# Performance work log

Hardware: AMD Instinct MI355X
Metric: run time of the kernel (lower is better)

## Reference

```python
import jax, jax.numpy as jnp
import numpy as np

H_DIM = 2048
D_FF = 4 * H_DIM
NUM_EXPERTS = 8
NUM_SHARED = 2
BATCH, SEQ = 2, 2048


def setup_inputs() -> dict:
    key = jax.random.key(0)
    ks = jax.random.split(key, 10)
    s = 0.02
    return {
        "x": jax.random.normal(ks[0], (BATCH, SEQ, H_DIM), dtype=jnp.float32),
        "ws_w1": jax.random.normal(ks[1], (NUM_SHARED, H_DIM, D_FF), dtype=jnp.float32) * s,
        "ws_b1": jnp.zeros((NUM_SHARED, D_FF), dtype=jnp.float32),
        "ws_w2": jax.random.normal(ks[2], (NUM_SHARED, D_FF, H_DIM), dtype=jnp.float32) * s,
        "ws_b2": jnp.zeros((NUM_SHARED, H_DIM), dtype=jnp.float32),
        "we_w1": jax.random.normal(ks[3], (NUM_EXPERTS, H_DIM, D_FF), dtype=jnp.float32) * s,
        "we_b1": jnp.zeros((NUM_EXPERTS, D_FF), dtype=jnp.float32),
        "we_w2": jax.random.normal(ks[4], (NUM_EXPERTS, D_FF, H_DIM), dtype=jnp.float32) * s,
        "we_b2": jnp.zeros((NUM_EXPERTS, H_DIM), dtype=jnp.float32),
        "wg": jax.random.normal(ks[5], (H_DIM, NUM_EXPERTS), dtype=jnp.float32) * s,
        "top_k": 2,
    }


def reference(x, ws_w1, ws_b1, ws_w2, ws_b2, we_w1, we_b1, we_w2, we_b2, wg, top_k):
    B, S, D = x.shape
    xt = x.reshape(-1, D)  # [T, D], T = B*S
    T = xt.shape[0]

    # ---- shared experts: sum over NUM_SHARED dense MLPs ----
    hs = jax.nn.relu(jnp.einsum('td,ndf->ntf', xt, ws_w1) + ws_b1[:, None, :])
    shared = jnp.einsum('ntf,nfd->td', hs, ws_w2) + ws_b2.sum(axis=0)  # [T, D]

    # ---- sparse top-k routed MoE ----
    logits = xt @ wg                       # [T, E] router logits
    probs = jax.nn.softmax(logits, axis=-1)
    topv, topi = jax.lax.top_k(probs, top_k)
    gates = jnp.zeros_like(probs).at[jnp.arange(T)[:, None], topi].set(topv)  # [T, E]

    moe = jnp.zeros_like(xt)
    for e in range(we_w1.shape[0]):  # small fixed expert count
        he = jax.nn.relu(xt @ we_w1[e] + we_b1[e])
        ye = he @ we_w2[e] + we_b2[e]
        moe = moe + gates[:, e:e + 1] * ye

    out = (shared + moe).reshape(B, S, D)
    return out, logits
```

## Files before the change

kernel.cpp:

```cpp
#include <hip/hip_runtime.h>

#define TOKENS 4096
#define HD 2048
#define FF 8192
#define NE 8
#define NS 2

typedef __attribute__((ext_vector_type(8))) short bf16x8;
typedef __attribute__((ext_vector_type(4))) float f32x4;

__device__ __forceinline__ unsigned rnd_bf(unsigned u) {
  return u + 0x7fffu + ((u >> 16) & 1u);
}
__device__ __forceinline__ unsigned short f2bf(float f) {
  unsigned u = __builtin_bit_cast(unsigned, f);
  return (unsigned short)(rnd_bf(u) >> 16);
}

#define GLDS16(gp, lp)                                                         \
  __builtin_amdgcn_global_load_lds(                                            \
      (const __attribute__((address_space(1))) unsigned*)(const void*)(gp),    \
      (__attribute__((address_space(3))) unsigned*)(lp), 16, 0, 0)

__global__ void cast_x_kernel(const float* __restrict__ x, unsigned short* __restrict__ xb) {
  const size_t i = ((size_t)blockIdx.x * 256 + threadIdx.x) * 4;
  float4 v = *(const float4*)(x + i);
  ushort4 o;
  o.x = f2bf(v.x); o.y = f2bf(v.y); o.z = f2bf(v.z); o.w = f2bf(v.w);
  *(ushort4*)(xb + i) = o;
}

__global__ void router_kernel(const float* __restrict__ x, const float* __restrict__ wg,
                              float* __restrict__ logits_out, int* __restrict__ topi,
                              float* __restrict__ topv, int* __restrict__ counts) {
  const int wave = threadIdx.x >> 6, lane = threadIdx.x & 63;
  const int t = blockIdx.x * 4 + wave;
  const float* xr = x + (size_t)t * HD;
  float acc[8];
#pragma unroll
  for (int e = 0; e < 8; ++e) acc[e] = 0.f;
  for (int d = lane; d < HD; d += 64) {
    const float xv = xr[d];
    const float4 w0 = *(const float4*)(wg + (size_t)d * 8);
    const float4 w1 = *(const float4*)(wg + (size_t)d * 8 + 4);
    acc[0] += xv * w0.x; acc[1] += xv * w0.y; acc[2] += xv * w0.z; acc[3] += xv * w0.w;
    acc[4] += xv * w1.x; acc[5] += xv * w1.y; acc[6] += xv * w1.z; acc[7] += xv * w1.w;
  }
#pragma unroll
  for (int e = 0; e < 8; ++e) {
#pragma unroll
    for (int off = 32; off > 0; off >>= 1) acc[e] += __shfl_xor(acc[e], off);
  }
  if (lane == 0) {
    *(float4*)(logits_out + (size_t)t * 8)     = make_float4(acc[0], acc[1], acc[2], acc[3]);
    *(float4*)(logits_out + (size_t)t * 8 + 4) = make_float4(acc[4], acc[5], acc[6], acc[7]);
    float mx = acc[0];
#pragma unroll
    for (int e = 1; e < 8; ++e) mx = fmaxf(mx, acc[e]);
    float p[8], s = 0.f;
#pragma unroll
    for (int e = 0; e < 8; ++e) { p[e] = expf(acc[e] - mx); s += p[e]; }
    const float inv = 1.f / s;
    int i1 = 0;
#pragma unroll
    for (int e = 1; e < 8; ++e) if (acc[e] > acc[i1]) i1 = e;
    int i2 = (i1 == 0) ? 1 : 0;
#pragma unroll
    for (int e = 0; e < 8; ++e) if (e != i1 && acc[e] > acc[i2]) i2 = e;
    topi[2 * t]     = i1; topv[2 * t]     = p[i1] * inv;
    topi[2 * t + 1] = i2; topv[2 * t + 1] = p[i2] * inv;
    atomicAdd(&counts[i1], 1);
    atomicAdd(&counts[i2], 1);
  }
}

__global__ void offs_kernel(const int* __restrict__ counts, int* __restrict__ offs,
                            int* __restrict__ cursors) {
  if (threadIdx.x == 0) {
    int r = 0;
    for (int e = 0; e < NE; ++e) { offs[e] = r; cursors[e] = r; r += counts[e]; }
  }
}

__global__ void gather_kernel(const unsigned short* __restrict__ xb,
                              const int* __restrict__ topi, const float* __restrict__ topv,
                              int* __restrict__ cursors, unsigned short* __restrict__ xg,
                              int* __restrict__ row_token, float* __restrict__ row_gate) {
  const int wave = threadIdx.x >> 6, lane = threadIdx.x & 63;
  const int t = blockIdx.x * 4 + wave;
  const uint4* src = (const uint4*)(xb + (size_t)t * HD);
#pragma unroll
  for (int j = 0; j < 2; ++j) {
    const int e = topi[2 * t + j];
    int pos = 0;
    if (lane == 0) {
      pos = atomicAdd(&cursors[e], 1);
      row_token[pos] = t;
      row_gate[pos] = topv[2 * t + j];
    }
    pos = __shfl(pos, 0);
    uint4* dst = (uint4*)(xg + (size_t)pos * HD);
#pragma unroll
    for (int c = lane; c < 256; c += 64) dst[c] = src[c];
  }
}

template <int K, int N>
__global__ __launch_bounds__(256) void pack_wt(const float* __restrict__ we,
                                               const float* __restrict__ ws,
                                               unsigned short* __restrict__ dstw) {
  const int e = blockIdx.z;
  const float* src = (e < NE) ? (we + (size_t)e * K * N) : (ws + (size_t)(e - NE) * K * N);
  unsigned short* dst = dstw + (size_t)e * K * N;
  const int nt = blockIdx.x * 64;
  const int kt = blockIdx.y * 64;
  __shared__ unsigned short t[64][73];
  const int tid = threadIdx.x;
  const int rr = tid >> 4, cc = (tid & 15) * 4;
#pragma unroll
  for (int i = 0; i < 4; ++i) {
    const int k = rr + i * 16;
    float4 v = *(const float4*)(src + (size_t)(kt + k) * N + nt + cc);
    t[k][cc + 0] = f2bf(v.x);
    t[k][cc + 1] = f2bf(v.y);
    t[k][cc + 2] = f2bf(v.z);
    t[k][cc + 3] = f2bf(v.w);
  }
  __syncthreads();
  const int nr = tid >> 2, kc = (tid & 3) * 16;
  unsigned u[8];
#pragma unroll
  for (int j = 0; j < 8; ++j)
    u[j] = (unsigned)t[kc + 2 * j][nr] | ((unsigned)t[kc + 2 * j + 1][nr] << 16);
  unsigned short* dp = dst + (size_t)(nt + nr) * K + kt + kc;
  uint4 v0; v0.x = u[0]; v0.y = u[1]; v0.z = u[2]; v0.w = u[3];
  uint4 v1; v1.x = u[4]; v1.y = u[5]; v1.z = u[6]; v1.w = u[7];
  *(uint4*)dp = v0;
  *(uint4*)(dp + 8) = v1;
}

template <int MS>
__device__ __forceinline__ void rd_a(bf16x8 (&d)[8], const unsigned short* base,
                                     int wr, int fr, int fq, int swz) {
#pragma unroll
  for (int mi = 0; mi < 4; ++mi)
#pragma unroll
    for (int ks = 0; ks < 2; ++ks)
      d[mi * 2 + ks] = *(const bf16x8*)(base + (wr * 128 + MS * 64 + mi * 16 + fr) * 64 +
                                        (((ks * 4 + fq) ^ swz) << 3));
}
template <int NSUB>
__device__ __forceinline__ void rd_b(bf16x8 (&d)[4], const unsigned short* base,
                                     int wc, int fr, int fq, int swz) {
#pragma unroll
  for (int ni = 0; ni < 2; ++ni)
#pragma unroll
    for (int ks = 0; ks < 2; ++ks)
      d[ni * 2 + ks] = *(const bf16x8*)(base + (wc * 64 + NSUB * 32 + ni * 16 + fr) * 64 +
                                        (((ks * 4 + fq) ^ swz) << 3));
}
template <int MS, int NSUB>
__device__ __forceinline__ void mm16(f32x4 (&acc)[8][4], const bf16x8 (&a)[8],
                                     const bf16x8 (&b)[4]) {
  __builtin_amdgcn_s_setprio(1);
#pragma unroll
  for (int mi = 0; mi < 4; ++mi)
#pragma unroll
    for (int ni = 0; ni < 2; ++ni)
#pragma unroll
      for (int ks = 0; ks < 2; ++ks)
        acc[MS * 4 + mi][NSUB * 2 + ni] = __builtin_amdgcn_mfma_f32_16x16x32_bf16(
            a[mi * 2 + ks], b[ni * 2 + ks], acc[MS * 4 + mi][NSUB * 2 + ni], 0, 0, 0);
  __builtin_amdgcn_s_setprio(0);
}

template <int MODE>
__global__ __launch_bounds__(512, 2) void gemm8p(
    const unsigned short* __restrict__ Ash,
    const unsigned short* __restrict__ Art,
    const unsigned short* __restrict__ wt,
    const float* __restrict__ bE, const float* __restrict__ bS,
    unsigned short* __restrict__ hout, float* __restrict__ out,
    const int* __restrict__ counts, const int* __restrict__ offs,
    const int* __restrict__ row_token, const float* __restrict__ row_gate) {
  constexpr int K = (MODE == 0) ? HD : FF;
  constexpr int N = (MODE == 0) ? FF : HD;
  constexpr int NBX = N / 256;
  constexpr int NWG = NBX * 16;
  extern __shared__ unsigned short smem[];

  const int e = blockIdx.z;
  int M;
  const unsigned short* A;
  const float* bias;
  int hbase = 0;
  const int* tok = nullptr;
  const float* gt = nullptr;

  if (e < NE) {
    M = counts[e];
    const int off = offs[e];
    A = Art + (size_t)off * K;
    if (MODE == 1) { tok = row_token + off; gt = row_gate + off; }
    bias = bE + (size_t)e * N;
    hbase = off;
  } else {
    M = TOKENS;
    const int se = e - NE;
    hbase = 2 * TOKENS + se * TOKENS;
    if (MODE == 0) A = Ash;
    else           A = Ash + (size_t)hbase * K;
    bias = bS + (size_t)se * N;
  }
  const unsigned short* Bt = wt + (size_t)e * HD * FF;

  int flat = blockIdx.x + NBX * blockIdx.y;
  flat = (flat & 7) * (NWG >> 3) + (flat >> 3);
  const int m0 = (flat & 15) * 256;
  const int n0 = (flat >> 4) * 256;
  if (m0 >= M) return;

  const int tid = threadIdx.x;
  const int wid = tid >> 6, ln = tid & 63;
  const int wr = wid >> 2, wc = wid & 3;
  const int fr = ln & 15, fq = ln >> 4;
  const int swz = fr & 7;

  const int srr = tid >> 3;
  const int soct = tid & 7;
  const int scol = (soct ^ (srr & 7)) << 3;

#define STAGE_A(h, kt, b)                                                      \
  { const unsigned short* s_ = A + (size_t)(m0 + (h) * 128 + srr) * K + (kt) * 64 + scol; \
    unsigned short* d_ = smem + (b) * 32768 + ((h) * 128 + srr) * 64 + soct * 8; \
    GLDS16(s_, d_); GLDS16(s_ + (size_t)64 * K, d_ + 4096); }
#define STAGE_B(h, kt, b)                                                      \
  { const unsigned short* s_ = Bt + (size_t)(n0 + (h) * 128 + srr) * K + (kt) * 64 + scol; \
    unsigned short* d_ = smem + (b) * 32768 + 16384 + ((h) * 128 + srr) * 64 + soct * 8; \
    GLDS16(s_, d_); GLDS16(s_ + (size_t)64 * K, d_ + 4096); }

  f32x4 acc[8][4];
#pragma unroll
  for (int i = 0; i < 8; ++i)
#pragma unroll
    for (int j = 0; j < 4; ++j) acc[i][j] = (f32x4){0.f, 0.f, 0.f, 0.f};

  STAGE_A(0, 0, 0); STAGE_B(0, 0, 0); STAGE_A(1, 0, 0); STAGE_B(1, 0, 0);
  STAGE_B(0, 1, 1); STAGE_A(0, 1, 1);
  asm volatile("s_waitcnt vmcnt(4)" ::: "memory");
  __builtin_amdgcn_s_barrier();

  bf16x8 a0[8], a1[8], b0[4], b1[4];
  const int nkt = K / 64;
  int cur = 0;
  for (int t = 0; t < nkt; ++t) {
    const int nxt = cur ^ 1;
    const int tp1 = (t + 1 < nkt) ? t + 1 : t;
    const int tp2 = (t + 2 < nkt) ? t + 2 : t;
    const unsigned short* As_c = smem + cur * 32768;
    const unsigned short* Bs_c = As_c + 16384;
    rd_a<0>(a0, As_c, wr, fr, fq, swz);
    rd_b<0>(b0, Bs_c, wc, fr, fq, swz);
    STAGE_A(1, tp1, nxt);
    __builtin_amdgcn_s_barrier();
    mm16<0, 0>(acc, a0, b0);
    __builtin_amdgcn_s_barrier();
    rd_b<1>(b1, Bs_c, wc, fr, fq, swz);
    STAGE_B(1, tp1, nxt);
    __builtin_amdgcn_s_barrier();
    mm16<0, 1>(acc, a0, b1);
    __builtin_amdgcn_s_barrier();
    rd_a<1>(a1, As_c, wr, fr, fq, swz);
    STAGE_B(0, tp2, cur);
    __builtin_amdgcn_s_barrier();
    mm16<1, 1>(acc, a1, b1);
    __builtin_amdgcn_s_barrier();
    STAGE_A(0, tp2, cur);
    __builtin_amdgcn_s_barrier();
    mm16<1, 0>(acc, a1, b0);
    asm volatile("s_waitcnt vmcnt(4)" ::: "memory");
    __builtin_amdgcn_s_barrier();
    cur = nxt;
  }
#undef STAGE_A
#undef STAGE_B

  if (MODE == 0) {
#pragma unroll
    for (int nn = 0; nn < 4; ++nn) {
      const int col = n0 + wc * 64 + (nn >> 1) * 32 + (nn & 1) * 16 + fr;
      const float bb = bias[col];
#pragma unroll
      for (int mm = 0; mm < 8; ++mm) {
#pragma unroll
        for (int j = 0; j < 4; ++j) {
          const int r = m0 + wr * 128 + (mm >> 2) * 64 + (mm & 3) * 16 + fq * 4 + j;
          if (r < M) {
            float v = acc[mm][nn][j] + bb;
            v = v > 0.f ? v : 0.f;
            hout[(size_t)(hbase + r) * FF + col] = f2bf(v);
          }
        }
      }
    }
  } else {
#pragma unroll
    for (int mm = 0; mm < 8; ++mm) {
#pragma unroll
      for (int j = 0; j < 4; ++j) {
        const int r = m0 + wr * 128 + (mm >> 2) * 64 + (mm & 3) * 16 + fq * 4 + j;
        if (r < M) {
          const int t = tok ? tok[r] : r;
          const float g = gt ? gt[r] : 1.f;
          float* orow = out + (size_t)t * HD + n0;
#pragma unroll
          for (int nn = 0; nn < 4; ++nn) {
            const int col = wc * 64 + (nn >> 1) * 32 + (nn & 1) * 16 + fr;
            atomicAdd(orow + col, g * (acc[mm][nn][j] + bias[n0 + col]));
          }
        }
      }
    }
  }
}

extern "C" void kernel_launch(void* const* d_in, const int* in_sizes, int n_in,
                              void* d_out, int out_size, void* d_ws, size_t ws_size,
                              hipStream_t stream) {
  const float* x     = (const float*)d_in[0];
  const float* ws_w1 = (const float*)d_in[1];
  const float* ws_b1 = (const float*)d_in[2];
  const float* ws_w2 = (const float*)d_in[3];
  const float* ws_b2 = (const float*)d_in[4];
  const float* we_w1 = (const float*)d_in[5];
  const float* we_b1 = (const float*)d_in[6];
  const float* we_w2 = (const float*)d_in[7];
  const float* we_b2 = (const float*)d_in[8];
  const float* wg    = (const float*)d_in[9];

  float* out = (float*)d_out;
  float* logits = out + (size_t)TOKENS * HD;

  char* ws = (char*)d_ws;
  unsigned short* wt   = (unsigned short*)ws;
  unsigned short* xb   = (unsigned short*)(ws + 335544320);
  unsigned short* xg   = (unsigned short*)(ws + 352321536);
  unsigned short* hbuf = (unsigned short*)(ws + 386400256);
  char* ctrl = ws + 654835712;
  int*   row_token = (int*)(ctrl);
  float* row_gate  = (float*)(ctrl + 32768);
  int*   topi      = (int*)(ctrl + 65536);
  float* topv      = (float*)(ctrl + 98304);
  int*   counts    = (int*)(ctrl + 131072);
  int*   offs      = (int*)(ctrl + 131104);
  int*   cursors   = (int*)(ctrl + 131136);

  hipFuncSetAttribute(reinterpret_cast<const void*>(gemm8p<0>),
                      hipFuncAttributeMaxDynamicSharedMemorySize, 131072);
  hipFuncSetAttribute(reinterpret_cast<const void*>(gemm8p<1>),
                      hipFuncAttributeMaxDynamicSharedMemorySize, 131072);

  hipMemsetAsync(out, 0, (size_t)TOKENS * HD * sizeof(float), stream);
  hipMemsetAsync(counts, 0, NE * sizeof(int), stream);

  cast_x_kernel<<<8192, 256, 0, stream>>>(x, xb);
  router_kernel<<<1024, 256, 0, stream>>>(x, wg, logits, topi, topv, counts);
  offs_kernel<<<1, 64, 0, stream>>>(counts, offs, cursors);
  gather_kernel<<<1024, 256, 0, stream>>>(xb, topi, topv, cursors, xg, row_token, row_gate);

  pack_wt<HD, FF><<<dim3(FF / 64, HD / 64, 10), 256, 0, stream>>>(we_w1, ws_w1, wt);
  gemm8p<0><<<dim3(32, 16, 10), 512, 131072, stream>>>(
      xb, xg, wt, we_b1, ws_b1, hbuf, nullptr, counts, offs, nullptr, nullptr);
  pack_wt<FF, HD><<<dim3(HD / 64, FF / 64, 10), 256, 0, stream>>>(we_w2, ws_w2, wt);
  gemm8p<1><<<dim3(8, 16, 10), 512, 131072, stream>>>(
      hbuf, hbuf, wt, we_b2, ws_b2, nullptr, out, counts, offs, row_token, row_gate);

  (void)in_sizes; (void)n_in; (void)out_size; (void)ws_size;
}
```

Before: 2.019 ms.

## Restage GEMM tiles per-wave with full two-tile-ahead prefetch pipeline

Changes how global-to-LDS loads are assigned: each wave now loads the rows it will itself read (wave-local row groups with 8-row strides), instead of a block-wide 128-row split. The prefetch schedule becomes uniform: both halves of A and B for tile t+2 are issued into the current buffer during compute of tile t, with a deeper vmcnt(8) wait. This aims to reduce cross-wave dependencies and smooth memory issue across the loop. The cost is more outstanding loads and registers, plus the risk of buffer overwrite hazards if the barriers do not fully cover reads of the current buffer.

```diff
diff --git a/kernel.cpp b/kernel.cpp
--- a/kernel.cpp
+++ b/kernel.cpp
@@ -226,18 +226,22 @@
   const int fr = ln & 15, fq = ln >> 4;
   const int swz = fr & 7;
 
-  const int srr = tid >> 3;
-  const int soct = tid & 7;
-  const int scol = (soct ^ (srr & 7)) << 3;
-
-#define STAGE_A(h, kt, b)                                                      \
-  { const unsigned short* s_ = A + (size_t)(m0 + (h) * 128 + srr) * K + (kt) * 64 + scol; \
-    unsigned short* d_ = smem + (b) * 32768 + ((h) * 128 + srr) * 64 + soct * 8; \
-    GLDS16(s_, d_); GLDS16(s_ + (size_t)64 * K, d_ + 4096); }
-#define STAGE_B(h, kt, b)                                                      \
-  { const unsigned short* s_ = Bt + (size_t)(n0 + (h) * 128 + srr) * K + (kt) * 64 + scol; \
-    unsigned short* d_ = smem + (b) * 32768 + 16384 + ((h) * 128 + srr) * 64 + soct * 8; \
-    GLDS16(s_, d_); GLDS16(s_ + (size_t)64 * K, d_ + 4096); }
+  const int lr8 = ln >> 3;
+  const int lc8 = ln & 7;
+  const int scol = (lc8 ^ lr8) << 3;
+  const int wrA = wr * 128 + wc * 16;
+  const int wcB = wc * 64 + wr * 16;
+
+#define SA(s, kt, b)                                                           \
+  { const int r0_ = wrA + (s) * 64 + lr8;                                      \
+    const unsigned short* s_ = A + (size_t)(m0 + r0_) * K + (kt) * 64 + scol;  \
+    unsigned short* d_ = smem + (b) * 32768 + r0_ * 64 + lc8 * 8;              \
+    GLDS16(s_, d_); GLDS16(s_ + (size_t)8 * K, d_ + 8 * 64); }
+#define SB(s, kt, b)                                                           \
+  { const int r0_ = wcB + (s) * 32 + lr8;                                      \
+    const unsigned short* s_ = Bt + (size_t)(n0 + r0_) * K + (kt) * 64 + scol; \
+    unsigned short* d_ = smem + (b) * 32768 + 16384 + r0_ * 64 + lc8 * 8;      \
+    GLDS16(s_, d_); GLDS16(s_ + (size_t)8 * K, d_ + 8 * 64); }
 
   f32x4 acc[8][4];
 #pragma unroll
@@ -245,45 +249,41 @@
 #pragma unroll
     for (int j = 0; j < 4; ++j) acc[i][j] = (f32x4){0.f, 0.f, 0.f, 0.f};
 
-  STAGE_A(0, 0, 0); STAGE_B(0, 0, 0); STAGE_A(1, 0, 0); STAGE_B(1, 0, 0);
-  STAGE_B(0, 1, 1); STAGE_A(0, 1, 1);
-  asm volatile("s_waitcnt vmcnt(4)" ::: "memory");
+  SA(0, 0, 0); SA(1, 0, 0); SB(0, 0, 0); SB(1, 0, 0);
+  SA(0, 1, 1); SA(1, 1, 1); SB(0, 1, 1); SB(1, 1, 1);
+  asm volatile("s_waitcnt vmcnt(8)" ::: "memory");
   __builtin_amdgcn_s_barrier();
 
   bf16x8 a0[8], a1[8], b0[4], b1[4];
   const int nkt = K / 64;
-  int cur = 0;
   for (int t = 0; t < nkt; ++t) {
-    const int nxt = cur ^ 1;
-    const int tp1 = (t + 1 < nkt) ? t + 1 : t;
+    const int cur = t & 1;
     const int tp2 = (t + 2 < nkt) ? t + 2 : t;
     const unsigned short* As_c = smem + cur * 32768;
     const unsigned short* Bs_c = As_c + 16384;
     rd_a<0>(a0, As_c, wr, fr, fq, swz);
     rd_b<0>(b0, Bs_c, wc, fr, fq, swz);
-    STAGE_A(1, tp1, nxt);
     __builtin_amdgcn_s_barrier();
     mm16<0, 0>(acc, a0, b0);
     __builtin_amdgcn_s_barrier();
     rd_b<1>(b1, Bs_c, wc, fr, fq, swz);
-    STAGE_B(1, tp1, nxt);
+    SA(0, tp2, cur); SB(0, tp2, cur);
     __builtin_amdgcn_s_barrier();
     mm16<0, 1>(acc, a0, b1);
     __builtin_amdgcn_s_barrier();
     rd_a<1>(a1, As_c, wr, fr, fq, swz);
-    STAGE_B(0, tp2, cur);
+    SB(1, tp2, cur);
     __builtin_amdgcn_s_barrier();
     mm16<1, 1>(acc, a1, b1);
     __builtin_amdgcn_s_barrier();
-    STAGE_A(0, tp2, cur);
+    SA(1, tp2, cur);
     __builtin_amdgcn_s_barrier();
     mm16<1, 0>(acc, a1, b0);
-    asm volatile("s_waitcnt vmcnt(4)" ::: "memory");
-    __builtin_amdgcn_s_barrier();
-    cur = nxt;
-  }
-#undef STAGE_A
-#undef STAGE_B
+    asm volatile("s_waitcnt vmcnt(8)" ::: "memory");
+    __builtin_amdgcn_s_barrier();
+  }
+#undef SA
+#undef SB
 
   if (MODE == 0) {
 #pragma unroll
```

Measured after the change: 2.073 ms. 2.7% more time.
